# Optimization experiments

Hardware: AMD Instinct MI355X
Metric: run time of the kernel (lower is better)

## Reference

```python
import jax, jax.numpy as jnp
import numpy as np

D_MODEL = 1024
N_HEADS = 16
D_K = D_MODEL // N_HEADS
B, S = 2, 2048


def setup_inputs() -> dict:
    key = jax.random.key(0)
    ks = jax.random.split(key, 8)
    scale = 1.0 / np.sqrt(D_MODEL)
    inp = {
        'query': jax.random.normal(ks[0], (B, S, D_MODEL), dtype=jnp.float32),
        'key':   jax.random.normal(ks[1], (B, S, D_MODEL), dtype=jnp.float32),
        'value': jax.random.normal(ks[2], (B, S, D_MODEL), dtype=jnp.float32),
        # causal mask: True = masked (matches masked_fill(mask == True, -1e9))
        'mask': jnp.triu(jnp.ones((1, 1, S, S), dtype=bool), k=1),
        'w_q': jax.random.normal(ks[3], (D_MODEL, D_MODEL), dtype=jnp.float32) * scale,
        'w_k': jax.random.normal(ks[4], (D_MODEL, D_MODEL), dtype=jnp.float32) * scale,
        'w_v': jax.random.normal(ks[5], (D_MODEL, D_MODEL), dtype=jnp.float32) * scale,
        'w_o': jax.random.normal(ks[6], (D_MODEL, D_MODEL), dtype=jnp.float32) * scale,
    }
    return inp


def reference(query, key, value, mask, w_q, w_k, w_v, w_o):
    # nn.Linear stores weight [out, in]; y = x @ W^T
    def split_heads(x, w):
        y = jnp.einsum('bsd,ed->bse', x, w)           # [B,S,D]
        return y.reshape(x.shape[0], x.shape[1], N_HEADS, D_K).transpose(0, 2, 1, 3)  # [B,H,S,dk]

    Q = split_heads(query, w_q)
    K = split_heads(key, w_k)
    V = split_heads(value, w_v)
    scores = jnp.einsum('bhqd,bhkd->bhqk', Q, K) / jnp.sqrt(jnp.float32(D_K))
    scores = jnp.where(mask, jnp.float32(-1e9), scores)
    attn = jax.nn.softmax(scores, axis=-1)            # dropout is identity in eval
    out = jnp.einsum('bhqk,bhkd->bhqd', attn, V)
    out = out.transpose(0, 2, 1, 3).reshape(query.shape[0], query.shape[1], D_MODEL)
    return jnp.einsum('bsd,ed->bse', out, w_o)
```

## Files before the change

kernel.cpp:

```cpp
#include <hip/hip_runtime.h>

#define D_MODEL 1024
#define NH 16
#define DK 64
#define BB 2
#define SS 2048
#define WELEMS (D_MODEL * D_MODEL)
#define XELEMS (BB * SS * D_MODEL)

typedef __attribute__((ext_vector_type(8))) short bf16x8;
typedef __attribute__((ext_vector_type(4))) float f32x4;
typedef __attribute__((ext_vector_type(4))) short s16x4;

__device__ __forceinline__ short f2bf(float f) {
    union { float f; unsigned u; } v; v.f = f;
    unsigned r = v.u + 0x7fffu + ((v.u >> 16) & 1u);
    return (short)(r >> 16);
}

__device__ __forceinline__ float fexp2(float x) {
    float r;
    asm("v_exp_f32 %0, %1" : "=v"(r) : "v"(x));
    return r;
}

__device__ __forceinline__ unsigned pkbf2(float hi, float lo) {
    union { float f; unsigned u; } a, b; a.f = hi; b.f = lo;
    return __builtin_amdgcn_perm(a.u + 0x8000u, b.u + 0x8000u, 0x07060302u);
}

#define AS1 __attribute__((address_space(1)))
#define AS3 __attribute__((address_space(3)))
__device__ __forceinline__ void glds16(const void* g, void* l) {
    __builtin_amdgcn_global_load_lds((AS1 const void*)g, (AS3 void*)l, 16, 0, 0);
}

__global__ __launch_bounds__(256) void convert_all(
    const float* __restrict__ wq, const float* __restrict__ wk,
    const float* __restrict__ wv, const float* __restrict__ wo,
    const float* __restrict__ qi, const float* __restrict__ ki,
    const float* __restrict__ vi, short* __restrict__ dst)
{
    size_t i = ((size_t)blockIdx.x * 256 + threadIdx.x) * 8;
    const float* src;
    size_t off;
    float sc = 1.0f;
    if (i < (size_t)4 * WELEMS) {
        int m = (int)(i >> 20);
        off = i & (WELEMS - 1);
        src = (m == 0) ? wq : (m == 1) ? wk : (m == 2) ? wv : wo;
        if (m == 0) sc = 0.125f * 1.44269504088896340736f;
    } else {
        size_t j = i - (size_t)4 * WELEMS;
        int a = (int)(j >> 22);
        off = j & (XELEMS - 1);
        src = (a == 0) ? qi : (a == 1) ? ki : vi;
    }
    float4 a = *(const float4*)(src + off);
    float4 b = *(const float4*)(src + off + 4);
    bf16x8 pk;
    pk[0] = f2bf(a.x * sc); pk[1] = f2bf(a.y * sc);
    pk[2] = f2bf(a.z * sc); pk[3] = f2bf(a.w * sc);
    pk[4] = f2bf(b.x * sc); pk[5] = f2bf(b.y * sc);
    pk[6] = f2bf(b.z * sc); pk[7] = f2bf(b.w * sc);
    *(bf16x8*)(dst + i) = pk;
}

__global__ __launch_bounds__(256) void qkv_gemm(
    const short* __restrict__ Xall, const short* __restrict__ Wall,
    short* __restrict__ Qo, short* __restrict__ Ko, short* __restrict__ Vo)
{
    const int z = blockIdx.z;
    const short* __restrict__ X = Xall + (size_t)z * XELEMS;
    const short* __restrict__ W = Wall + (size_t)z * WELEMS;

    __shared__ short As[128 * 64];
    __shared__ short Bs[128 * 64];

    const int tid = threadIdx.x;
    const int w = tid >> 6, lane = tid & 63;
    const int l15 = lane & 15, quad = lane >> 4;
    const int wrow = (w >> 1) * 64, wcol = (w & 1) * 64;
    const int m0 = blockIdx.x * 128, n0 = blockIdx.y * 128;
    const int br = lane >> 3, bc = lane & 7;

    f32x4 acc[4][4];
    #pragma unroll
    for (int i = 0; i < 4; ++i)
        #pragma unroll
        for (int j = 0; j < 4; ++j) acc[i][j] = (f32x4){0.f, 0.f, 0.f, 0.f};

    for (int k0 = 0; k0 < D_MODEL; k0 += 64) {
        __syncthreads();
        #pragma unroll
        for (int i = 0; i < 4; ++i) {
            int r = (w * 4 + i) * 8 + br;
            int g = bc ^ (r & 7);
            glds16(X + (size_t)(m0 + r) * D_MODEL + k0 + g * 8, &As[(w * 4 + i) * 512]);
            glds16(W + (size_t)(n0 + r) * D_MODEL + k0 + g * 8, &Bs[(w * 4 + i) * 512]);
        }
        __syncthreads();

        #pragma unroll
        for (int kk = 0; kk < 2; ++kk) {
            const int swz = l15 & 7;
            bf16x8 af[4], bfr[4];
            #pragma unroll
            for (int i = 0; i < 4; ++i) {
                int row = wrow + i * 16 + l15;
                af[i] = *(const bf16x8*)&As[row * 64 + (((kk * 4 + quad) ^ swz) * 8)];
            }
            #pragma unroll
            for (int j = 0; j < 4; ++j) {
                int col = wcol + j * 16 + l15;
                bfr[j] = *(const bf16x8*)&Bs[col * 64 + (((kk * 4 + quad) ^ swz) * 8)];
            }
            #pragma unroll
            for (int i = 0; i < 4; ++i)
                #pragma unroll
                for (int j = 0; j < 4; ++j)
                    acc[i][j] = __builtin_amdgcn_mfma_f32_16x16x32_bf16(af[i], bfr[j], acc[i][j], 0, 0, 0);
        }
    }

    if (z < 2) {
        short* O = z ? Ko : Qo;
        #pragma unroll
        for (int i = 0; i < 4; ++i) {
            int m = m0 + wrow + i * 16 + quad * 4;
            #pragma unroll
            for (int j = 0; j < 4; ++j) {
                int n = n0 + wcol + j * 16 + l15;
                #pragma unroll
                for (int r = 0; r < 4; ++r)
                    O[(size_t)(m + r) * D_MODEL + n] = f2bf(acc[i][j][r]);
            }
        }
    } else {
        const int mbase = m0 + wrow;
        const int b = mbase >> 11, sbase = mbase & (SS - 1);
        #pragma unroll
        for (int j = 0; j < 4; ++j) {
            int n = n0 + wcol + j * 16 + l15;
            int h = n >> 6, d = n & 63;
            short* vdst = Vo + (((size_t)(b * NH + h)) * DK + d) * SS + sbase + quad * 16;
            #pragma unroll
            for (int r = 0; r < 4; ++r) {
                uint2 pk;
                pk.x = pkbf2(acc[1][j][r], acc[0][j][r]);
                pk.y = pkbf2(acc[3][j][r], acc[2][j][r]);
                *(uint2*)(vdst + r * 4) = pk;
            }
        }
    }
}

__global__ __launch_bounds__(256) void attn(
    const short* __restrict__ Q, const short* __restrict__ K,
    const short* __restrict__ V, short* __restrict__ O)
{
    const int h = blockIdx.y, b = blockIdx.z;
    const int tid = threadIdx.x, w = tid >> 6, lane = tid & 63;
    const int l15 = lane & 15, quad = lane >> 4;

    __shared__ short Ks[2][64 * 64];
    __shared__ short Vs[2][64 * 64];
    __shared__ short Ps[4][16 * 64];

    const size_t qk_base = ((size_t)b * SS) * D_MODEL + h * DK;
    const short* Kh = K + qk_base;
    const short* Vh = V + ((size_t)(b * NH + h)) * DK * SS;

    const int grow = lane >> 3;
    const int gchunk = (lane & 7) ^ (grow & 7);
    const int wv2 = w & 1;
    const short* stK = Kh + (size_t)(wv2 * 32 + grow) * D_MODEL + gchunk * 8;
    const short* stV = Vh + (size_t)(wv2 * 32 + grow) * SS + gchunk * 8;

    short* const pw = &Ps[w][0];
    const int pswz = l15 & 7;

    for (int half = 0; half < 2; ++half) {
        const int qt = half ? (31 - blockIdx.x) : blockIdx.x;

        bf16x8 qf0, qf1;
        {
            const short* qp = Q + qk_base + (size_t)(qt * 64 + w * 16 + l15) * D_MODEL;
            qf0 = *(const bf16x8*)(qp + quad * 8);
            qf1 = *(const bf16x8*)(qp + 32 + quad * 8);
        }

        f32x4 oacc[4];
        #pragma unroll
        for (int c = 0; c < 4; ++c) oacc[c] = (f32x4){0.f, 0.f, 0.f, 0.f};
        float lsum[4] = {0.f, 0.f, 0.f, 0.f};

        __syncthreads();
        if (w < 2) {
            #pragma unroll
            for (int i = 0; i < 4; ++i)
                glds16(stK + (size_t)i * 8 * D_MODEL, &Ks[0][(wv2 * 32 + i * 8) * 64]);
        } else {
            #pragma unroll
            for (int i = 0; i < 4; ++i)
                glds16(stV + (size_t)i * 8 * SS, &Vs[0][(wv2 * 32 + i * 8) * 64]);
        }

        int buf = 0;
        for (int kt = 0; kt <= qt; ++kt) {
            __syncthreads();
            if (kt < qt) {
                const int nb = buf ^ 1;
                if (w < 2) {
                    #pragma unroll
                    for (int i = 0; i < 4; ++i)
                        glds16(stK + (size_t)((kt + 1) * 64 + i * 8) * D_MODEL,
                               &Ks[nb][(wv2 * 32 + i * 8) * 64]);
                } else {
                    #pragma unroll
                    for (int i = 0; i < 4; ++i)
                        glds16(stV + (size_t)(i * 8) * SS + (kt + 1) * 64,
                               &Vs[nb][(wv2 * 32 + i * 8) * 64]);
                }
            }

            const short* ksb = &Ks[buf][0];
            const short* vsb = &Vs[buf][0];

            f32x4 sacc[4];
            #pragma unroll
            for (int c = 0; c < 4; ++c) sacc[c] = (f32x4){0.f, 0.f, 0.f, 0.f};
            #pragma unroll
            for (int c = 0; c < 4; ++c) {
                int krow = c * 16 + l15, ksw = krow & 7;
                bf16x8 b0 = *(const bf16x8*)&ksb[krow * 64 + ((quad ^ ksw) * 8)];
                bf16x8 b1 = *(const bf16x8*)&ksb[krow * 64 + (((4 + quad) ^ ksw) * 8)];
                sacc[c] = __builtin_amdgcn_mfma_f32_16x16x32_bf16(qf0, b0, sacc[c], 0, 0, 0);
                sacc[c] = __builtin_amdgcn_mfma_f32_16x16x32_bf16(qf1, b1, sacc[c], 0, 0, 0);
            }

            float pv_[4][4];
            if (kt == qt) {
                const int gq = w * 16 + quad * 4;
                #pragma unroll
                for (int c = 0; c < 4; ++c) {
                    int ck = c * 16 + l15;
                    #pragma unroll
                    for (int r = 0; r < 4; ++r)
                        pv_[c][r] = (ck <= gq + r) ? fexp2(sacc[c][r]) : 0.f;
                }
            } else {
                #pragma unroll
                for (int c = 0; c < 4; ++c)
                    #pragma unroll
                    for (int r = 0; r < 4; ++r)
                        pv_[c][r] = fexp2(sacc[c][r]);
            }
            #pragma unroll
            for (int r = 0; r < 4; ++r)
                lsum[r] += (pv_[0][r] + pv_[1][r]) + (pv_[2][r] + pv_[3][r]);

            #pragma unroll
            for (int r = 0; r < 4; ++r) {
                int prow = quad * 4 + r;
                int pchunk = (l15 >> 1) ^ (prow & 7);
                uint2 pk;
                pk.x = pkbf2(pv_[1][r], pv_[0][r]);
                pk.y = pkbf2(pv_[3][r], pv_[2][r]);
                *(uint2*)&pw[prow * 64 + pchunk * 8 + (l15 & 1) * 4] = pk;
            }

            #pragma unroll
            for (int kk = 0; kk < 2; ++kk) {
                int u = kk * 4 + quad;
                bf16x8 pf = *(const bf16x8*)&pw[l15 * 64 + ((u ^ pswz) * 8)];
                #pragma unroll
                for (int c = 0; c < 4; ++c) {
                    int vrow = c * 16 + l15;
                    bf16x8 vf = *(const bf16x8*)&vsb[vrow * 64 + ((u ^ (vrow & 7)) * 8)];
                    oacc[c] = __builtin_amdgcn_mfma_f32_16x16x32_bf16(pf, vf, oacc[c], 0, 0, 0);
                }
            }
            buf ^= 1;
        }

        #pragma unroll
        for (int r = 0; r < 4; ++r) {
            float s = lsum[r];
            s += __shfl_xor(s, 1, 64); s += __shfl_xor(s, 2, 64);
            s += __shfl_xor(s, 4, 64); s += __shfl_xor(s, 8, 64);
            lsum[r] = 1.f / s;
        }
        const size_t obase = ((size_t)b * SS + qt * 64 + w * 16 + quad * 4) * D_MODEL + h * DK;
        #pragma unroll
        for (int r = 0; r < 4; ++r)
            #pragma unroll
            for (int c = 0; c < 4; ++c)
                O[obase + (size_t)r * D_MODEL + c * 16 + l15] = f2bf(oacc[c][r] * lsum[r]);
    }
}

__global__ __launch_bounds__(256) void out_gemm(
    const short* __restrict__ A, const short* __restrict__ W,
    float* __restrict__ C)
{
    __shared__ short As[128 * 64];
    __shared__ short Bs[64 * 64];

    const int tid = threadIdx.x;
    const int w = tid >> 6, lane = tid & 63;
    const int l15 = lane & 15, quad = lane >> 4;
    const int wrow = w * 32;
    const int m0 = blockIdx.x * 128, n0 = blockIdx.y * 64;
    const int br = lane >> 3, bc = lane & 7;

    f32x4 acc[2][4];
    #pragma unroll
    for (int i = 0; i < 2; ++i)
        #pragma unroll
        for (int j = 0; j < 4; ++j) acc[i][j] = (f32x4){0.f, 0.f, 0.f, 0.f};

    for (int k0 = 0; k0 < D_MODEL; k0 += 64) {
        __syncthreads();
        #pragma unroll
        for (int i = 0; i < 4; ++i) {
            int r = (w * 4 + i) * 8 + br;
            int g = bc ^ (r & 7);
            glds16(A + (size_t)(m0 + r) * D_MODEL + k0 + g * 8, &As[(w * 4 + i) * 512]);
        }
        #pragma unroll
        for (int i = 0; i < 2; ++i) {
            int r = (w * 2 + i) * 8 + br;
            int g = bc ^ (r & 7);
            glds16(W + (size_t)(n0 + r) * D_MODEL + k0 + g * 8, &Bs[(w * 2 + i) * 512]);
        }
        __syncthreads();

        #pragma unroll
        for (int kk = 0; kk < 2; ++kk) {
            const int swz = l15 & 7;
            bf16x8 af[2], bfr[4];
            #pragma unroll
            for (int i = 0; i < 2; ++i) {
                int row = wrow + i * 16 + l15;
                af[i] = *(const bf16x8*)&As[row * 64 + (((kk * 4 + quad) ^ swz) * 8)];
            }
            #pragma unroll
            for (int j = 0; j < 4; ++j) {
                int col = j * 16 + l15;
                bfr[j] = *(const bf16x8*)&Bs[col * 64 + (((kk * 4 + quad) ^ swz) * 8)];
            }
            #pragma unroll
            for (int i = 0; i < 2; ++i)
                #pragma unroll
                for (int j = 0; j < 4; ++j)
                    acc[i][j] = __builtin_amdgcn_mfma_f32_16x16x32_bf16(af[i], bfr[j], acc[i][j], 0, 0, 0);
        }
    }

    #pragma unroll
    for (int i = 0; i < 2; ++i) {
        int m = m0 + wrow + i * 16 + quad * 4;
        #pragma unroll
        for (int j = 0; j < 4; ++j) {
            int n = n0 + j * 16 + l15;
            #pragma unroll
            for (int r = 0; r < 4; ++r)
                C[(size_t)(m + r) * D_MODEL + n] = acc[i][j][r];
        }
    }
}

extern "C" void kernel_launch(void* const* d_in, const int* in_sizes, int n_in,
                              void* d_out, int out_size, void* d_ws, size_t ws_size,
                              hipStream_t stream) {
    const float* q  = (const float*)d_in[0];
    const float* k  = (const float*)d_in[1];
    const float* v  = (const float*)d_in[2];
    const float* wq = (const float*)d_in[4];
    const float* wk = (const float*)d_in[5];
    const float* wv = (const float*)d_in[6];
    const float* wo = (const float*)d_in[7];

    short* wbf = (short*)d_ws;
    short* xbf = wbf + 4 * (size_t)WELEMS;
    short* Qb  = xbf + 3 * (size_t)XELEMS;
    short* Kb  = Qb + (size_t)XELEMS;
    short* Vb  = Kb + (size_t)XELEMS;
    short* Ob  = Qb;

    const int conv_elems = 4 * WELEMS + 3 * XELEMS;
    convert_all<<<dim3(conv_elems / (256 * 8)), 256, 0, stream>>>(
        wq, wk, wv, wo, q, k, v, wbf);
    qkv_gemm<<<dim3(32, 8, 3), 256, 0, stream>>>(xbf, wbf, Qb, Kb, Vb);
    attn<<<dim3(16, NH, BB), 256, 0, stream>>>(Qb, Kb, Vb, Ob);
    out_gemm<<<dim3(32, 16), 256, 0, stream>>>(Ob, wbf + 3 * (size_t)WELEMS, (float*)d_out);
}
```

Before: 209.6 us.

## Software-pipeline PV MFMA one tile behind QK in attention loop

Restructures the attention inner loop so the P·V product for the previous key tile runs right after the current tile's QK^T MFMAs, before the exp and P store. V gets a triple buffer and P a per-warp double buffer, and a final PV step drains the last tile after the loop. The goal is to overlap the MFMA work with the softmax ALU and LDS write latency, and to remove the dependency stall between writing P and reading it back. The cost is extra LDS and more register pressure, which could reduce occupancy.

```diff
diff --git a/kernel.cpp b/kernel.cpp
--- a/kernel.cpp
+++ b/kernel.cpp
@@ -164,8 +164,8 @@
     const int l15 = lane & 15, quad = lane >> 4;
 
     __shared__ short Ks[2][64 * 64];
-    __shared__ short Vs[2][64 * 64];
-    __shared__ short Ps[4][16 * 64];
+    __shared__ short Vs[3][64 * 64];
+    __shared__ short Ps[4][2][16 * 64];
 
     const size_t qk_base = ((size_t)b * SS) * D_MODEL + h * DK;
     const short* Kh = K + qk_base;
@@ -177,7 +177,6 @@
     const short* stK = Kh + (size_t)(wv2 * 32 + grow) * D_MODEL + gchunk * 8;
     const short* stV = Vh + (size_t)(wv2 * 32 + grow) * SS + gchunk * 8;
 
-    short* const pw = &Ps[w][0];
     const int pswz = l15 & 7;
 
     for (int half = 0; half < 2; ++half) {
@@ -206,26 +205,26 @@
                 glds16(stV + (size_t)i * 8 * SS, &Vs[0][(wv2 * 32 + i * 8) * 64]);
         }
 
-        int buf = 0;
+        int kcur = 0, vcur = 0;
         for (int kt = 0; kt <= qt; ++kt) {
             __syncthreads();
             if (kt < qt) {
-                const int nb = buf ^ 1;
+                const int knb = kcur ^ 1;
+                const int vnb = (vcur == 2) ? 0 : vcur + 1;
                 if (w < 2) {
                     #pragma unroll
                     for (int i = 0; i < 4; ++i)
                         glds16(stK + (size_t)((kt + 1) * 64 + i * 8) * D_MODEL,
-                               &Ks[nb][(wv2 * 32 + i * 8) * 64]);
+                               &Ks[knb][(wv2 * 32 + i * 8) * 64]);
                 } else {
                     #pragma unroll
                     for (int i = 0; i < 4; ++i)
                         glds16(stV + (size_t)(i * 8) * SS + (kt + 1) * 64,
-                               &Vs[nb][(wv2 * 32 + i * 8) * 64]);
+                               &Vs[vnb][(wv2 * 32 + i * 8) * 64]);
                 }
             }
 
-            const short* ksb = &Ks[buf][0];
-            const short* vsb = &Vs[buf][0];
+            const short* ksb = &Ks[kcur][0];
 
             f32x4 sacc[4];
             #pragma unroll
@@ -237,6 +236,23 @@
                 bf16x8 b1 = *(const bf16x8*)&ksb[krow * 64 + (((4 + quad) ^ ksw) * 8)];
                 sacc[c] = __builtin_amdgcn_mfma_f32_16x16x32_bf16(qf0, b0, sacc[c], 0, 0, 0);
                 sacc[c] = __builtin_amdgcn_mfma_f32_16x16x32_bf16(qf1, b1, sacc[c], 0, 0, 0);
+            }
+
+            if (kt > 0) {
+                int vprev = vcur + 2; if (vprev >= 3) vprev -= 3;
+                const short* vsb = &Vs[vprev][0];
+                const short* pp = &Ps[w][(kt - 1) & 1][0];
+                #pragma unroll
+                for (int kk = 0; kk < 2; ++kk) {
+                    int u = kk * 4 + quad;
+                    bf16x8 pf = *(const bf16x8*)&pp[l15 * 64 + ((u ^ pswz) * 8)];
+                    #pragma unroll
+                    for (int c = 0; c < 4; ++c) {
+                        int vrow = c * 16 + l15;
+                        bf16x8 vf = *(const bf16x8*)&vsb[vrow * 64 + ((u ^ (vrow & 7)) * 8)];
+                        oacc[c] = __builtin_amdgcn_mfma_f32_16x16x32_bf16(pf, vf, oacc[c], 0, 0, 0);
+                    }
+                }
             }
 
             float pv_[4][4];
@@ -260,20 +276,31 @@
             for (int r = 0; r < 4; ++r)
                 lsum[r] += (pv_[0][r] + pv_[1][r]) + (pv_[2][r] + pv_[3][r]);
 
-            #pragma unroll
-            for (int r = 0; r < 4; ++r) {
-                int prow = quad * 4 + r;
-                int pchunk = (l15 >> 1) ^ (prow & 7);
-                uint2 pk;
-                pk.x = pkbf2(pv_[1][r], pv_[0][r]);
-                pk.y = pkbf2(pv_[3][r], pv_[2][r]);
-                *(uint2*)&pw[prow * 64 + pchunk * 8 + (l15 & 1) * 4] = pk;
-            }
-
+            {
+                short* pw = &Ps[w][kt & 1][0];
+                #pragma unroll
+                for (int r = 0; r < 4; ++r) {
+                    int prow = quad * 4 + r;
+                    int pchunk = (l15 >> 1) ^ (prow & 7);
+                    uint2 pk;
+                    pk.x = pkbf2(pv_[1][r], pv_[0][r]);
+                    pk.y = pkbf2(pv_[3][r], pv_[2][r]);
+                    *(uint2*)&pw[prow * 64 + pchunk * 8 + (l15 & 1) * 4] = pk;
+                }
+            }
+
+            kcur ^= 1;
+            vcur = (vcur == 2) ? 0 : vcur + 1;
+        }
+
+        {
+            int vq = vcur + 2; if (vq >= 3) vq -= 3;
+            const short* vsb = &Vs[vq][0];
+            const short* pp = &Ps[w][qt & 1][0];
             #pragma unroll
             for (int kk = 0; kk < 2; ++kk) {
                 int u = kk * 4 + quad;
-                bf16x8 pf = *(const bf16x8*)&pw[l15 * 64 + ((u ^ pswz) * 8)];
+                bf16x8 pf = *(const bf16x8*)&pp[l15 * 64 + ((u ^ pswz) * 8)];
                 #pragma unroll
                 for (int c = 0; c < 4; ++c) {
                     int vrow = c * 16 + l15;
@@ -281,7 +308,6 @@
                     oacc[c] = __builtin_amdgcn_mfma_f32_16x16x32_bf16(pf, vf, oacc[c], 0, 0, 0);
                 }
             }
-            buf ^= 1;
         }
 
         #pragma unroll
```

Measured after the change: 211.5 us. Within noise of the previous version (+0.9%).

## Process paired causal query tiles concurrently in one 512-thread block sharing K/V tiles

Applied to the files above, without the earlier changes.

The attention kernel used to process two query tiles (x and 31-x) one after the other in a 256-thread block. It now launches 512 threads, with each group of 4 waves owning one of the two query tiles. Both groups share a single K/V streaming pass up to the longer tile's limit, so K/V loads are halved and each wave issues fewer tile loads. The cost is that the short tile's waves sit idle at barriers for the later iterations, and the block's resource footprint grows.

```diff
diff --git a/kernel.cpp b/kernel.cpp
--- a/kernel.cpp
+++ b/kernel.cpp
@@ -155,17 +155,22 @@
     }
 }
 
-__global__ __launch_bounds__(256) void attn(
+__global__ __launch_bounds__(512) void attn(
     const short* __restrict__ Q, const short* __restrict__ K,
     const short* __restrict__ V, short* __restrict__ O)
 {
+    const int x = blockIdx.x;
     const int h = blockIdx.y, b = blockIdx.z;
     const int tid = threadIdx.x, w = tid >> 6, lane = tid & 63;
     const int l15 = lane & 15, quad = lane >> 4;
+    const int grp = w >> 2;
+    const int wg = w & 3;
+    const int qt = grp ? (31 - x) : x;
+    const int ktmax = 31 - x;
 
     __shared__ short Ks[2][64 * 64];
     __shared__ short Vs[2][64 * 64];
-    __shared__ short Ps[4][16 * 64];
+    __shared__ short Ps[8][16 * 64];
 
     const size_t qk_base = ((size_t)b * SS) * D_MODEL + h * DK;
     const short* Kh = K + qk_base;
@@ -173,57 +178,53 @@
 
     const int grow = lane >> 3;
     const int gchunk = (lane & 7) ^ (grow & 7);
-    const int wv2 = w & 1;
-    const short* stK = Kh + (size_t)(wv2 * 32 + grow) * D_MODEL + gchunk * 8;
-    const short* stV = Vh + (size_t)(wv2 * 32 + grow) * SS + gchunk * 8;
+    const short* stK = Kh + (size_t)(wg * 16 + grow) * D_MODEL + gchunk * 8;
+    const short* stV = Vh + (size_t)(wg * 16 + grow) * SS + gchunk * 8;
 
     short* const pw = &Ps[w][0];
     const int pswz = l15 & 7;
 
-    for (int half = 0; half < 2; ++half) {
-        const int qt = half ? (31 - blockIdx.x) : blockIdx.x;
-
-        bf16x8 qf0, qf1;
-        {
-            const short* qp = Q + qk_base + (size_t)(qt * 64 + w * 16 + l15) * D_MODEL;
-            qf0 = *(const bf16x8*)(qp + quad * 8);
-            qf1 = *(const bf16x8*)(qp + 32 + quad * 8);
-        }
-
-        f32x4 oacc[4];
-        #pragma unroll
-        for (int c = 0; c < 4; ++c) oacc[c] = (f32x4){0.f, 0.f, 0.f, 0.f};
-        float lsum[4] = {0.f, 0.f, 0.f, 0.f};
-
-        __syncthreads();
-        if (w < 2) {
-            #pragma unroll
-            for (int i = 0; i < 4; ++i)
-                glds16(stK + (size_t)i * 8 * D_MODEL, &Ks[0][(wv2 * 32 + i * 8) * 64]);
-        } else {
-            #pragma unroll
-            for (int i = 0; i < 4; ++i)
-                glds16(stV + (size_t)i * 8 * SS, &Vs[0][(wv2 * 32 + i * 8) * 64]);
-        }
-
-        int buf = 0;
-        for (int kt = 0; kt <= qt; ++kt) {
-            __syncthreads();
-            if (kt < qt) {
-                const int nb = buf ^ 1;
-                if (w < 2) {
-                    #pragma unroll
-                    for (int i = 0; i < 4; ++i)
-                        glds16(stK + (size_t)((kt + 1) * 64 + i * 8) * D_MODEL,
-                               &Ks[nb][(wv2 * 32 + i * 8) * 64]);
-                } else {
-                    #pragma unroll
-                    for (int i = 0; i < 4; ++i)
-                        glds16(stV + (size_t)(i * 8) * SS + (kt + 1) * 64,
-                               &Vs[nb][(wv2 * 32 + i * 8) * 64]);
-                }
-            }
-
+    bf16x8 qf0, qf1;
+    {
+        const short* qp = Q + qk_base + (size_t)(qt * 64 + wg * 16 + l15) * D_MODEL;
+        qf0 = *(const bf16x8*)(qp + quad * 8);
+        qf1 = *(const bf16x8*)(qp + 32 + quad * 8);
+    }
+
+    f32x4 oacc[4];
+    #pragma unroll
+    for (int c = 0; c < 4; ++c) oacc[c] = (f32x4){0.f, 0.f, 0.f, 0.f};
+    float lsum[4] = {0.f, 0.f, 0.f, 0.f};
+
+    if (grp == 0) {
+        #pragma unroll
+        for (int i = 0; i < 2; ++i)
+            glds16(stK + (size_t)i * 8 * D_MODEL, &Ks[0][(wg * 16 + i * 8) * 64]);
+    } else {
+        #pragma unroll
+        for (int i = 0; i < 2; ++i)
+            glds16(stV + (size_t)i * 8 * SS, &Vs[0][(wg * 16 + i * 8) * 64]);
+    }
+
+    int buf = 0;
+    for (int kt = 0; kt <= ktmax; ++kt) {
+        __syncthreads();
+        if (kt < ktmax) {
+            const int nb = buf ^ 1;
+            if (grp == 0) {
+                #pragma unroll
+                for (int i = 0; i < 2; ++i)
+                    glds16(stK + (size_t)((kt + 1) * 64 + i * 8) * D_MODEL,
+                           &Ks[nb][(wg * 16 + i * 8) * 64]);
+            } else {
+                #pragma unroll
+                for (int i = 0; i < 2; ++i)
+                    glds16(stV + (size_t)(i * 8) * SS + (kt + 1) * 64,
+                           &Vs[nb][(wg * 16 + i * 8) * 64]);
+            }
+        }
+
+        if (kt <= qt) {
             const short* ksb = &Ks[buf][0];
             const short* vsb = &Vs[buf][0];
 
@@ -241,7 +242,7 @@
 
             float pv_[4][4];
             if (kt == qt) {
-                const int gq = w * 16 + quad * 4;
+                const int gq = wg * 16 + quad * 4;
                 #pragma unroll
                 for (int c = 0; c < 4; ++c) {
                     int ck = c * 16 + l15;
@@ -281,23 +282,23 @@
                     oacc[c] = __builtin_amdgcn_mfma_f32_16x16x32_bf16(pf, vf, oacc[c], 0, 0, 0);
                 }
             }
-            buf ^= 1;
-        }
-
-        #pragma unroll
-        for (int r = 0; r < 4; ++r) {
-            float s = lsum[r];
-            s += __shfl_xor(s, 1, 64); s += __shfl_xor(s, 2, 64);
-            s += __shfl_xor(s, 4, 64); s += __shfl_xor(s, 8, 64);
-            lsum[r] = 1.f / s;
-        }
-        const size_t obase = ((size_t)b * SS + qt * 64 + w * 16 + quad * 4) * D_MODEL + h * DK;
-        #pragma unroll
-        for (int r = 0; r < 4; ++r)
-            #pragma unroll
-            for (int c = 0; c < 4; ++c)
-                O[obase + (size_t)r * D_MODEL + c * 16 + l15] = f2bf(oacc[c][r] * lsum[r]);
-    }
+        }
+        buf ^= 1;
+    }
+
+    #pragma unroll
+    for (int r = 0; r < 4; ++r) {
+        float s = lsum[r];
+        s += __shfl_xor(s, 1, 64); s += __shfl_xor(s, 2, 64);
+        s += __shfl_xor(s, 4, 64); s += __shfl_xor(s, 8, 64);
+        lsum[r] = 1.f / s;
+    }
+    const size_t obase = ((size_t)b * SS + qt * 64 + wg * 16 + quad * 4) * D_MODEL + h * DK;
+    #pragma unroll
+    for (int r = 0; r < 4; ++r)
+        #pragma unroll
+        for (int c = 0; c < 4; ++c)
+            O[obase + (size_t)r * D_MODEL + c * 16 + l15] = f2bf(oacc[c][r] * lsum[r]);
 }
 
 __global__ __launch_bounds__(256) void out_gemm(
@@ -393,6 +394,6 @@
     convert_all<<<dim3(conv_elems / (256 * 8)), 256, 0, stream>>>(
         wq, wk, wv, wo, q, k, v, wbf);
     qkv_gemm<<<dim3(32, 8, 3), 256, 0, stream>>>(xbf, wbf, Qb, Kb, Vb);
-    attn<<<dim3(16, NH, BB), 256, 0, stream>>>(Qb, Kb, Vb, Ob);
+    attn<<<dim3(16, NH, BB), 512, 0, stream>>>(Qb, Kb, Vb, Ob);
     out_gemm<<<dim3(32, 16), 256, 0, stream>>>(Ob, wbf + 3 * (size_t)WELEMS, (float*)d_out);
 }
```

Measured after the change: 204.4 us. 1.03x faster.
